# Optimization experiments

Hardware: AMD Instinct MI355X
Metric: run time of the kernel (lower is better)

Reference implementation:

```python
import jax, jax.numpy as jnp
import numpy as np

DECAY = 0.999
EPS = 1e-06
NUM_CLUSTERS = 512
NUM_HEADS = 8
DIM_PER_HEAD = 64


def setup_inputs() -> dict:
    key = jax.random.key(0)
    k1, k2 = jax.random.split(key)
    x = jax.random.normal(k1, (8, 2048, NUM_HEADS * DIM_PER_HEAD), dtype=jnp.float32)
    means = jax.random.normal(k2, (NUM_HEADS, NUM_CLUSTERS, DIM_PER_HEAD), dtype=jnp.float32)
    return {"x": x, "means": means}


def reference(x, means):
    b, n, _ = x.shape
    h, k, d = means.shape
    xh = x.reshape(b, n, h, d)  # 'b n (h d) -> b n h d'
    dists = (
        jnp.sum(xh ** 2, axis=-1)[..., None]
        - 2.0 * jnp.einsum('bnhd,hkd->bnhk', xh, means)
        + jnp.sum(means ** 2, axis=-1)[None, None, :, :]
    )
    cluster_ids = jnp.argmin(dists, axis=-1)  # [b, n, h] int
    # training-path EMA codebook update
    one_hot = jax.nn.one_hot(cluster_ids, k, dtype=jnp.float32)  # [b, n, h, k]
    per_cluster_count = jnp.sum(one_hot, axis=(0, 1))  # [h, k]
    sum_x = jnp.einsum('bnhk,bnhd->hkd', one_hot, xh)  # [h, k, d]
    new_means = sum_x / (EPS + per_cluster_count[..., None])
    updated_means = (1.0 - DECAY) * new_means + DECAY * means
    return cluster_ids, updated_means
```

## Files before the change

kernel.cpp:

```cpp
#include <hip/hip_runtime.h>

#define NUM_HEADS 8
#define DIM 64
#define NCLUST 512
#define NTOK 16384
#define ROWLEN 512
#define NIDS (NTOK * NUM_HEADS)
#define NMEANS (NUM_HEADS * NCLUST * DIM)
#define NCK (NUM_HEADS * NCLUST)
#define TPB 64
#define KQ 128
#define CAP 16
#define DELTA 0.35f

typedef unsigned long long u64;
typedef short bf16x8 __attribute__((ext_vector_type(8)));
typedef float f32x4 __attribute__((ext_vector_type(4)));

__device__ __forceinline__ unsigned short f2bf(float f) {
    unsigned b = __float_as_uint(f);
    return (unsigned short)((b + 0x7fffu + ((b >> 16) & 1u)) >> 16);
}
__device__ __forceinline__ unsigned pack2bf(float lo, float hi) {
    return (unsigned)f2bf(lo) | ((unsigned)f2bf(hi) << 16);
}
__device__ __forceinline__ float bf2f(unsigned short b) {
    return __uint_as_float((unsigned)b << 16);
}
__device__ __forceinline__ u64 packkey(float s, int k) {
    unsigned u = __float_as_uint(s);
    unsigned ord = (u & 0x80000000u) ? ~u : (u | 0x80000000u);
    return ((u64)(~ord) << 32) | (unsigned)k;
}
__device__ __forceinline__ int swz(int row, int byte_in_row) {
    return row * 128 + (byte_in_row ^ ((row & 7) << 4));
}

__global__ void vq_prep(const float* __restrict__ means,
                        float* __restrict__ q,
                        unsigned short* __restrict__ mbf) {
    int g = blockIdx.x * blockDim.x + threadIdx.x;
    int row = g >> 4, c = g & 15;
    float4 v = *(const float4*)(means + (size_t)row * DIM + c * 4);
    ushort4 b;
    b.x = f2bf(v.x); b.y = f2bf(v.y); b.z = f2bf(v.z); b.w = f2bf(v.w);
    *(ushort4*)(mbf + (size_t)row * DIM + c * 4) = b;
    float s = fmaf(v.x, v.x, fmaf(v.y, v.y, fmaf(v.z, v.z, v.w * v.w)));
#pragma unroll
    for (int off = 1; off < 16; off <<= 1) s += __shfl_xor(s, off, 64);
    if (c == 0) q[row] = 0.5f * s;
}

__global__ __launch_bounds__(256, 4) void vq_score(const float* __restrict__ x,
                                                   const float* __restrict__ means,
                                                   const unsigned short* __restrict__ mbf,
                                                   const float* __restrict__ q,
                                                   float* __restrict__ ids_f) {
    __shared__ __align__(16) unsigned char msq[KQ * 128];
    __shared__ float qs[NCLUST];
    __shared__ int cnt[TPB];
    __shared__ unsigned short candL[TPB][CAP];

    const int head = blockIdx.y;
    const int t0   = blockIdx.x * TPB;
    const int tid  = threadIdx.x;
    const int wv = tid >> 6, l = tid & 63;
    const int lg = l >> 4, lc = l & 15;
    const int twave = wv * 16;

    auto stage_async = [&](int qt) {
        const unsigned char* gbase = (const unsigned char*)mbf
            + ((size_t)head * NCLUST + (size_t)qt * KQ) * (DIM * 2);
        const int rloc = l >> 3;
        const int srcb = ((l & 7) << 4) ^ (rloc << 4);
#pragma unroll
        for (int i = 0; i < 4; ++i) {
            int chunk = wv * 4 + i;
            const unsigned char* src = gbase + (chunk * 8 + rloc) * 128 + srcb;
            __builtin_amdgcn_global_load_lds(
                (const __attribute__((address_space(1))) unsigned int*)src,
                (__attribute__((address_space(3))) unsigned int*)(msq + chunk * 1024),
                16, 0, 0);
        }
    };

    bf16x8 af[2];
    {
        const float* xrow = x + (size_t)(t0 + twave + lc) * ROWLEN + head * DIM;
#pragma unroll
        for (int ks = 0; ks < 2; ++ks) {
            float av[8];
            *(float4*)&av[0] = *(const float4*)(xrow + ks * 32 + lg * 8);
            *(float4*)&av[4] = *(const float4*)(xrow + ks * 32 + lg * 8 + 4);
#pragma unroll
            for (int j = 0; j < 8; ++j) af[ks][j] = (short)f2bf(av[j]);
        }
    }
    qs[tid] = q[head * NCLUST + tid];
    qs[tid + 256] = q[head * NCLUST + tid + 256];
    if (tid < TPB) cnt[tid] = 0;
    stage_async(0);
    __syncthreads();

    float best[4];
#pragma unroll
    for (int r = 0; r < 4; ++r) best[r] = -3.0e38f;

    for (int qt = 0; qt < 4; ++qt) {
        f32x4 A[8];
#pragma unroll
        for (int ct = 0; ct < 8; ++ct) {
            bf16x8 b0 = *(const bf16x8*)(msq + swz(ct * 16 + lc, 0 + lg * 16));
            bf16x8 b1 = *(const bf16x8*)(msq + swz(ct * 16 + lc, 64 + lg * 16));
            float qv = qs[qt * KQ + ct * 16 + lc];
            f32x4 acc = (f32x4){-qv, -qv, -qv, -qv};
            acc = __builtin_amdgcn_mfma_f32_16x16x32_bf16(af[0], b0, acc, 0, 0, 0);
            acc = __builtin_amdgcn_mfma_f32_16x16x32_bf16(af[1], b1, acc, 0, 0, 0);
            A[ct] = acc;
        }
        __syncthreads();
        if (qt < 3) stage_async(qt + 1);

#pragma unroll
        for (int ct = 0; ct < 8; ++ct)
#pragma unroll
            for (int r = 0; r < 4; ++r) best[r] = fmaxf(best[r], A[ct][r]);
        float thr[4];
#pragma unroll
        for (int r = 0; r < 4; ++r) {
#pragma unroll
            for (int off = 1; off < 16; off <<= 1)
                best[r] = fmaxf(best[r], __shfl_xor(best[r], off, 64));
            thr[r] = best[r] - DELTA;
        }
#pragma unroll
        for (int ct = 0; ct < 8; ++ct) {
            int k = qt * KQ + ct * 16 + lc;
#pragma unroll
            for (int r = 0; r < 4; ++r) {
                if (A[ct][r] >= thr[r]) {
                    int tok = twave + lg * 4 + r;
                    int slot = atomicAdd(&cnt[tok], 1);
                    if (slot < CAP) candL[tok][slot] = (unsigned short)k;
                }
            }
        }
        __syncthreads();
    }

#pragma unroll
    for (int g = 0; g < 4; ++g) {
        int tok = twave + g * 4 + lg;
        int n = cnt[tok];
        const float4 xv = *(const float4*)(x + (size_t)(t0 + tok) * ROWLEN + head * DIM + lc * 4);
        u64 bk = ~0ull;
        if (n > CAP) {
            for (int k = 0; k < NCLUST; ++k) {
                const float4 mv = *(const float4*)(means + ((size_t)head * NCLUST + k) * DIM + lc * 4);
                float p = fmaf(xv.x, mv.x, fmaf(xv.y, mv.y, fmaf(xv.z, mv.z, xv.w * mv.w)));
#pragma unroll
                for (int off = 1; off < 16; off <<= 1) p += __shfl_xor(p, off, 64);
                u64 cd = packkey(p - qs[k], k);
                bk = cd < bk ? cd : bk;
            }
        } else {
            for (int j = 0; j < n; ++j) {
                int k = candL[tok][j];
                const float4 mv = *(const float4*)(means + ((size_t)head * NCLUST + k) * DIM + lc * 4);
                float p = fmaf(xv.x, mv.x, fmaf(xv.y, mv.y, fmaf(xv.z, mv.z, xv.w * mv.w)));
#pragma unroll
                for (int off = 1; off < 16; off <<= 1) p += __shfl_xor(p, off, 64);
                u64 cd = packkey(p - qs[k], k);
                bk = cd < bk ? cd : bk;
            }
        }
        if (lc == 0) ids_f[(size_t)(t0 + tok) * NUM_HEADS + head] = (float)(unsigned)(bk & 0x1ffu);
    }
}

__global__ void vq_scatter(const float* __restrict__ x,
                           const float* __restrict__ ids_f,
                           float* __restrict__ counts,
                           unsigned short* __restrict__ sums_bf,
                           int rep_mask) {
    int g = blockIdx.x * blockDim.x + threadIdx.x;
    int p = g >> 5;
    int l32 = threadIdx.x & 31;
    int token = p >> 3;
    int h = p & 7;
    int rep = token & rep_mask;
    int id = (int)ids_f[p];
    float2 xv = *(const float2*)(x + (size_t)token * ROWLEN + h * DIM + l32 * 2);
    unsigned val = pack2bf(xv.x, xv.y);
    unsigned short* dst = sums_bf + (size_t)rep * NMEANS
                        + (((size_t)h * NCLUST + id) << 6) + l32 * 2;
    asm volatile("global_atomic_pk_add_bf16 %0, %1, off" :: "v"(dst), "v"(val) : "memory");
    if (l32 == 0) atomicAdd(&counts[rep * NCK + h * NCLUST + id], 1.0f);
}

__global__ void vq_final(const float* __restrict__ means,
                         const float* __restrict__ counts,
                         const unsigned short* __restrict__ sums_bf,
                         float* __restrict__ out_means,
                         int nrep) {
    int i = blockIdx.x * blockDim.x + threadIdx.x;
    int ck = i >> 6;
    float c = 0.f, s = 0.f;
    for (int r = 0; r < nrep; ++r) {
        c += counts[r * NCK + ck];
        s += bf2f(sums_bf[(size_t)r * NMEANS + i]);
    }
    float nm = s / (1e-6f + c);
    out_means[i] = 0.999f * means[i] + 0.001f * nm;
}

extern "C" void kernel_launch(void* const* d_in, const int* in_sizes, int n_in,
                              void* d_out, int out_size, void* d_ws, size_t ws_size,
                              hipStream_t stream) {
    const float* x     = (const float*)d_in[0];
    const float* means = (const float*)d_in[1];

    float* out       = (float*)d_out;
    float* ids_f     = out;
    float* out_means = out + NIDS;

    float*          q   = (float*)d_ws;
    unsigned short* mbf = (unsigned short*)(q + NCK);
    float*          fbase = (float*)(mbf + NMEANS);
    size_t core = (size_t)((char*)fbase - (char*)d_ws);

    size_t per_rep = (size_t)NCK * sizeof(float) + (size_t)NMEANS * sizeof(unsigned short);
    int nrep = 1;
    for (int r = 8; r > 1; r >>= 1) {
        if (ws_size >= core + (size_t)r * per_rep) { nrep = r; break; }
    }
    float*          counts  = fbase;
    unsigned short* sums_bf = (unsigned short*)(counts + (size_t)nrep * NCK);

    hipMemsetAsync(counts, 0, (size_t)nrep * per_rep, stream);

    vq_prep<<<(NCK * 16) / 256, 256, 0, stream>>>(means, q, mbf);

    dim3 gs(NTOK / TPB, NUM_HEADS);
    vq_score<<<gs, 256, 0, stream>>>(x, means, mbf, q, ids_f);

    vq_scatter<<<(NIDS * 32) / 256, 256, 0, stream>>>(x, ids_f, counts, sums_bf, nrep - 1);

    vq_final<<<NMEANS / 256, 256, 0, stream>>>(means, counts, sums_bf, out_means, nrep);
}
```

Measured before the change: 84.70 us.

## Stage whole per-head codebook in LDS and process more tokens per block

```diff
diff --git a/kernel.cpp b/kernel.cpp
--- a/kernel.cpp
+++ b/kernel.cpp
@@ -8,9 +8,7 @@
 #define NIDS (NTOK * NUM_HEADS)
 #define NMEANS (NUM_HEADS * NCLUST * DIM)
 #define NCK (NUM_HEADS * NCLUST)
-#define TPB 64
-#define KQ 128
-#define CAP 16
+#define CAP 8
 #define DELTA 0.35f
 
 typedef unsigned long long u64;
@@ -51,130 +49,140 @@
     if (c == 0) q[row] = 0.5f * s;
 }
 
-__global__ __launch_bounds__(256, 4) void vq_score(const float* __restrict__ x,
+__global__ __launch_bounds__(256, 2) void vq_score(const float* __restrict__ x,
                                                    const float* __restrict__ means,
                                                    const unsigned short* __restrict__ mbf,
                                                    const float* __restrict__ q,
                                                    float* __restrict__ ids_f) {
-    __shared__ __align__(16) unsigned char msq[KQ * 128];
+    __shared__ __align__(16) unsigned char msq[NCLUST * 128];
     __shared__ float qs[NCLUST];
-    __shared__ int cnt[TPB];
-    __shared__ unsigned short candL[TPB][CAP];
-
-    const int head = blockIdx.y;
-    const int t0   = blockIdx.x * TPB;
+    __shared__ int cnt[4][32];
+    __shared__ unsigned short candL[4][32][CAP];
+
+    const int head = blockIdx.x >> 6;
+    const int bloc = blockIdx.x & 63;
     const int tid  = threadIdx.x;
     const int wv = tid >> 6, l = tid & 63;
     const int lg = l >> 4, lc = l & 15;
-    const int twave = wv * 16;
-
-    auto stage_async = [&](int qt) {
+    const int wg = bloc * 4 + wv;
+    const int tile0 = wg * 4;
+
+    {
         const unsigned char* gbase = (const unsigned char*)mbf
-            + ((size_t)head * NCLUST + (size_t)qt * KQ) * (DIM * 2);
+            + (size_t)head * NCLUST * (DIM * 2);
         const int rloc = l >> 3;
         const int srcb = ((l & 7) << 4) ^ (rloc << 4);
 #pragma unroll
-        for (int i = 0; i < 4; ++i) {
-            int chunk = wv * 4 + i;
+        for (int i = 0; i < 16; ++i) {
+            int chunk = wv * 16 + i;
             const unsigned char* src = gbase + (chunk * 8 + rloc) * 128 + srcb;
             __builtin_amdgcn_global_load_lds(
                 (const __attribute__((address_space(1))) unsigned int*)src,
                 (__attribute__((address_space(3))) unsigned int*)(msq + chunk * 1024),
                 16, 0, 0);
         }
-    };
-
-    bf16x8 af[2];
-    {
-        const float* xrow = x + (size_t)(t0 + twave + lc) * ROWLEN + head * DIM;
+    }
+    qs[tid] = q[head * NCLUST + tid];
+    qs[tid + 256] = q[head * NCLUST + tid + 256];
+
+    bf16x8 af[4][2];
+#pragma unroll
+    for (int t = 0; t < 4; ++t) {
+        const float* xrow = x + (size_t)((tile0 + t) * 16 + lc) * ROWLEN + head * DIM;
 #pragma unroll
         for (int ks = 0; ks < 2; ++ks) {
             float av[8];
             *(float4*)&av[0] = *(const float4*)(xrow + ks * 32 + lg * 8);
             *(float4*)&av[4] = *(const float4*)(xrow + ks * 32 + lg * 8 + 4);
 #pragma unroll
-            for (int j = 0; j < 8; ++j) af[ks][j] = (short)f2bf(av[j]);
-        }
-    }
-    qs[tid] = q[head * NCLUST + tid];
-    qs[tid + 256] = q[head * NCLUST + tid + 256];
-    if (tid < TPB) cnt[tid] = 0;
-    stage_async(0);
+            for (int j = 0; j < 8; ++j) af[t][ks][j] = (short)f2bf(av[j]);
+        }
+    }
     __syncthreads();
 
-    float best[4];
-#pragma unroll
-    for (int r = 0; r < 4; ++r) best[r] = -3.0e38f;
-
-    for (int qt = 0; qt < 4; ++qt) {
-        f32x4 A[8];
-#pragma unroll
-        for (int ct = 0; ct < 8; ++ct) {
+    for (int ps = 0; ps < 2; ++ps) {
+        const int ta = ps * 2;
+        if (l < 32) cnt[wv][l] = 0;
+
+        float best[2][4];
+#pragma unroll
+        for (int tt = 0; tt < 2; ++tt)
+#pragma unroll
+            for (int r = 0; r < 4; ++r) best[tt][r] = -3.0e38f;
+
+        for (int ct = 0; ct < 32; ++ct) {
             bf16x8 b0 = *(const bf16x8*)(msq + swz(ct * 16 + lc, 0 + lg * 16));
             bf16x8 b1 = *(const bf16x8*)(msq + swz(ct * 16 + lc, 64 + lg * 16));
-            float qv = qs[qt * KQ + ct * 16 + lc];
-            f32x4 acc = (f32x4){-qv, -qv, -qv, -qv};
-            acc = __builtin_amdgcn_mfma_f32_16x16x32_bf16(af[0], b0, acc, 0, 0, 0);
-            acc = __builtin_amdgcn_mfma_f32_16x16x32_bf16(af[1], b1, acc, 0, 0, 0);
-            A[ct] = acc;
-        }
-        __syncthreads();
-        if (qt < 3) stage_async(qt + 1);
-
-#pragma unroll
-        for (int ct = 0; ct < 8; ++ct)
-#pragma unroll
-            for (int r = 0; r < 4; ++r) best[r] = fmaxf(best[r], A[ct][r]);
-        float thr[4];
-#pragma unroll
-        for (int r = 0; r < 4; ++r) {
-#pragma unroll
-            for (int off = 1; off < 16; off <<= 1)
-                best[r] = fmaxf(best[r], __shfl_xor(best[r], off, 64));
-            thr[r] = best[r] - DELTA;
-        }
-#pragma unroll
-        for (int ct = 0; ct < 8; ++ct) {
-            int k = qt * KQ + ct * 16 + lc;
+            float qv = qs[ct * 16 + lc];
+#pragma unroll
+            for (int tt = 0; tt < 2; ++tt) {
+                f32x4 acc = (f32x4){-qv, -qv, -qv, -qv};
+                acc = __builtin_amdgcn_mfma_f32_16x16x32_bf16(af[ta + tt][0], b0, acc, 0, 0, 0);
+                acc = __builtin_amdgcn_mfma_f32_16x16x32_bf16(af[ta + tt][1], b1, acc, 0, 0, 0);
+#pragma unroll
+                for (int r = 0; r < 4; ++r) best[tt][r] = fmaxf(best[tt][r], acc[r]);
+            }
+        }
+        float thr[2][4];
+#pragma unroll
+        for (int tt = 0; tt < 2; ++tt)
 #pragma unroll
             for (int r = 0; r < 4; ++r) {
-                if (A[ct][r] >= thr[r]) {
-                    int tok = twave + lg * 4 + r;
-                    int slot = atomicAdd(&cnt[tok], 1);
-                    if (slot < CAP) candL[tok][slot] = (unsigned short)k;
+#pragma unroll
+                for (int off = 1; off < 16; off <<= 1)
+                    best[tt][r] = fmaxf(best[tt][r], __shfl_xor(best[tt][r], off, 64));
+                thr[tt][r] = best[tt][r] - DELTA;
+            }
+
+        for (int ct = 0; ct < 32; ++ct) {
+            bf16x8 b0 = *(const bf16x8*)(msq + swz(ct * 16 + lc, 0 + lg * 16));
+            bf16x8 b1 = *(const bf16x8*)(msq + swz(ct * 16 + lc, 64 + lg * 16));
+            float qv = qs[ct * 16 + lc];
+            int k = ct * 16 + lc;
+#pragma unroll
+            for (int tt = 0; tt < 2; ++tt) {
+                f32x4 acc = (f32x4){-qv, -qv, -qv, -qv};
+                acc = __builtin_amdgcn_mfma_f32_16x16x32_bf16(af[ta + tt][0], b0, acc, 0, 0, 0);
+                acc = __builtin_amdgcn_mfma_f32_16x16x32_bf16(af[ta + tt][1], b1, acc, 0, 0, 0);
+#pragma unroll
+                for (int r = 0; r < 4; ++r) {
+                    if (acc[r] >= thr[tt][r]) {
+                        int tl = tt * 16 + lg * 4 + r;
+                        int slot = atomicAdd(&cnt[wv][tl], 1);
+                        if (slot < CAP) candL[wv][tl][slot] = (unsigned short)k;
+                    }
                 }
             }
         }
-        __syncthreads();
-    }
-
-#pragma unroll
-    for (int g = 0; g < 4; ++g) {
-        int tok = twave + g * 4 + lg;
-        int n = cnt[tok];
-        const float4 xv = *(const float4*)(x + (size_t)(t0 + tok) * ROWLEN + head * DIM + lc * 4);
-        u64 bk = ~0ull;
-        if (n > CAP) {
-            for (int k = 0; k < NCLUST; ++k) {
-                const float4 mv = *(const float4*)(means + ((size_t)head * NCLUST + k) * DIM + lc * 4);
-                float p = fmaf(xv.x, mv.x, fmaf(xv.y, mv.y, fmaf(xv.z, mv.z, xv.w * mv.w)));
-#pragma unroll
-                for (int off = 1; off < 16; off <<= 1) p += __shfl_xor(p, off, 64);
-                u64 cd = packkey(p - qs[k], k);
-                bk = cd < bk ? cd : bk;
-            }
-        } else {
-            for (int j = 0; j < n; ++j) {
-                int k = candL[tok][j];
-                const float4 mv = *(const float4*)(means + ((size_t)head * NCLUST + k) * DIM + lc * 4);
-                float p = fmaf(xv.x, mv.x, fmaf(xv.y, mv.y, fmaf(xv.z, mv.z, xv.w * mv.w)));
-#pragma unroll
-                for (int off = 1; off < 16; off <<= 1) p += __shfl_xor(p, off, 64);
-                u64 cd = packkey(p - qs[k], k);
-                bk = cd < bk ? cd : bk;
-            }
-        }
-        if (lc == 0) ids_f[(size_t)(t0 + tok) * NUM_HEADS + head] = (float)(unsigned)(bk & 0x1ffu);
+
+        for (int g = 0; g < 8; ++g) {
+            int tl = g * 4 + lg;
+            int token = (tile0 + ps * 2 + (tl >> 4)) * 16 + (tl & 15);
+            int n = cnt[wv][tl];
+            const float4 xv = *(const float4*)(x + (size_t)token * ROWLEN + head * DIM + lc * 4);
+            u64 bk = ~0ull;
+            if (n > CAP) {
+                for (int k = 0; k < NCLUST; ++k) {
+                    const float4 mv = *(const float4*)(means + ((size_t)head * NCLUST + k) * DIM + lc * 4);
+                    float p = fmaf(xv.x, mv.x, fmaf(xv.y, mv.y, fmaf(xv.z, mv.z, xv.w * mv.w)));
+#pragma unroll
+                    for (int off = 1; off < 16; off <<= 1) p += __shfl_xor(p, off, 64);
+                    u64 cd = packkey(p - qs[k], k);
+                    bk = cd < bk ? cd : bk;
+                }
+            } else {
+                for (int j = 0; j < n; ++j) {
+                    int k = candL[wv][tl][j];
+                    const float4 mv = *(const float4*)(means + ((size_t)head * NCLUST + k) * DIM + lc * 4);
+                    float p = fmaf(xv.x, mv.x, fmaf(xv.y, mv.y, fmaf(xv.z, mv.z, xv.w * mv.w)));
+#pragma unroll
+                    for (int off = 1; off < 16; off <<= 1) p += __shfl_xor(p, off, 64);
+                    u64 cd = packkey(p - qs[k], k);
+                    bk = cd < bk ? cd : bk;
+                }
+            }
+            if (lc == 0) ids_f[(size_t)token * NUM_HEADS + head] = (float)(unsigned)(bk & 0x1ffu);
+        }
     }
 }
 
@@ -241,8 +249,7 @@
 
     vq_prep<<<(NCK * 16) / 256, 256, 0, stream>>>(means, q, mbf);
 
-    dim3 gs(NTOK / TPB, NUM_HEADS);
-    vq_score<<<gs, 256, 0, stream>>>(x, means, mbf, q, ids_f);
+    vq_score<<<NUM_HEADS * 64, 256, 0, stream>>>(x, means, mbf, q, ids_f);
 
     vq_scatter<<<(NIDS * 32) / 256, 256, 0, stream>>>(x, ids_f, counts, sums_bf, nrep - 1);
 
```

After: 140.3 us. +65.6%, slower.
